# Kernel tuning notes

Measured on AMD Instinct MI355X. Metric: run time of the kernel, lower is better.

## Reference

```python
import jax, jax.numpy as jnp
import numpy as np

N = 400_000      # total nodes in batched graph
E = 6_400_000    # total edges (avg degree 16)
G = 6_400        # total small graphs
B = 64           # samples; num[i] graphs per sample, sum(num)=G
F = 31           # feature dim (hard-coded in TAG)
K = 2            # TAGConv hops
L = 5            # number of TAGConv layers
MAXG = 120       # max graphs per sample (120*31 pad)


def setup_inputs() -> dict:
    key = jax.random.key(0)
    ks = jax.random.split(key, 8)
    x = jax.random.normal(ks[0], (N, F), dtype=jnp.float32)
    src = jax.random.randint(ks[1], (E,), 0, N, dtype=jnp.int32)
    dst = jax.random.randint(ks[2], (E,), 0, N, dtype=jnp.int32)
    # contiguous (sorted) graph assignment, every graph non-empty (~62 nodes each)
    graph_ids = jnp.asarray((np.arange(N, dtype=np.int64) * G) // N, dtype=jnp.int32)
    num = jnp.full((B,), G // B, dtype=jnp.int32)  # 100 graphs per sample
    Ws = jax.random.normal(ks[3], (L, (K + 1) * F, F), dtype=jnp.float32) * 0.1
    bs = jax.random.normal(ks[4], (L, F), dtype=jnp.float32) * 0.01
    w_gate = jax.random.normal(ks[5], (F,), dtype=jnp.float32) * 0.1
    b_gate = jax.random.normal(ks[6], (1,), dtype=jnp.float32) * 0.01
    return {"x": x, "Ws": Ws, "bs": bs, "w_gate": w_gate, "b_gate": b_gate,
            "src": src, "dst": dst, "graph_ids": graph_ids, "num": num}


def reference(x, Ws, bs, w_gate, b_gate, src, dst, graph_ids, num):
    # symmetric normalization: norm = in_deg^{-1/2}, deg clamped to >=1 (DGL TAGConv)
    deg = jax.ops.segment_sum(jnp.ones((E,), x.dtype), dst, num_segments=N)
    norm = jnp.clip(deg, 1.0, None) ** -0.5  # [N]

    def tagconv(h, W, b):
        fstack = [h]
        cur = h
        for _ in range(K):
            cur = norm[:, None] * cur
            cur = jax.ops.segment_sum(cur[src], dst, num_segments=N)  # SPMM hop
            cur = norm[:, None] * cur
            fstack.append(cur)
        return jnp.concatenate(fstack, axis=-1) @ W + b  # [N, F]

    h = x
    for l in range(L):
        h = jax.nn.relu(tagconv(h, Ws[l], bs[l]))

    # GlobalAttentionPooling: segment softmax over gate scores, weighted sum
    gate = h @ w_gate + b_gate[0]                                   # [N]
    gmax = jax.ops.segment_max(gate, graph_ids, num_segments=G)     # [G]
    e = jnp.exp(gate - gmax[graph_ids])
    den = jax.ops.segment_sum(e, graph_ids, num_segments=G)
    alpha = e / den[graph_ids]
    rep = jax.ops.segment_sum(alpha[:, None] * h, graph_ids, num_segments=G)  # [G, F]

    # split by num, flatten, pad to 120*31, stack
    csum = jnp.cumsum(num)
    offsets = jnp.concatenate([jnp.zeros((1,), jnp.int32), csum.astype(jnp.int32)])
    g = jnp.arange(G, dtype=jnp.int32)
    sample_id = jnp.searchsorted(csum, g, side="right").astype(jnp.int32)  # [G]
    pos = g - offsets[sample_id]
    out = jnp.zeros((B, MAXG, F), rep.dtype).at[sample_id, pos].set(rep)
    return out.reshape(B, MAXG * F)
```

## Files before the change

### kernel.cpp

```cpp
#include <hip/hip_runtime.h>
#include <hip/hip_bf16.h>

#define FDIM 31
#define FPAD 32
#define RSTRIDE 16

#define CBITS 11
#define CW    (1 << CBITS)
#define MAXBUK 256
#define TILE 4096

typedef int      iv4 __attribute__((ext_vector_type(4)));
typedef unsigned uv4 __attribute__((ext_vector_type(4)));

__device__ __forceinline__ float bf_lo(unsigned u) { return __uint_as_float(u << 16); }
__device__ __forceinline__ float bf_hi(unsigned u) { return __uint_as_float(u & 0xFFFF0000u); }
__device__ __forceinline__ unsigned pack2(float lo, float hi) {
    unsigned a = __float_as_uint(lo), b = __float_as_uint(hi);
    unsigned ra = (a + 0x7FFFu + ((a >> 16) & 1u)) >> 16;
    unsigned rb = (b + 0x7FFFu + ((b >> 16) & 1u)) >> 16;
    return ra | (rb << 16);
}

__device__ __forceinline__ int lb_gid(const int* __restrict__ gid, int Ntot, int g) {
    int lo = 0, hi = Ntot;
    while (lo < hi) { int mid = (lo + hi) >> 1; if (gid[mid] < g) lo = mid + 1; else hi = mid; }
    return lo;
}

__global__ __launch_bounds__(256) void multisplit_kernel(
    const int* __restrict__ src, const int* __restrict__ dst,
    int* __restrict__ gcnt, int* __restrict__ bucketed,
    int cap, int E, int nbuk)
{
    __shared__ int ordered[TILE];
    __shared__ int hist[MAXBUK];
    __shared__ int lofs[MAXBUK + 1];
    __shared__ int base_[MAXBUK];
    __shared__ int cur[MAXBUK];
    const int tid = threadIdx.x;
    const int e0 = blockIdx.x * TILE;
    const int n = min(TILE, E - e0);
    if (tid < MAXBUK) hist[tid] = 0;
    __syncthreads();
    for (int i = tid; i < n; i += 256)
        atomicAdd(&hist[dst[e0 + i] >> CBITS], 1);
    __syncthreads();
    if (tid == 0) {
        int a = 0;
        for (int b = 0; b < nbuk; ++b) { lofs[b] = a; a += hist[b]; }
        lofs[nbuk] = a;
    }
    __syncthreads();
    if (tid < nbuk) {
        int h = hist[tid];
        base_[tid] = h ? atomicAdd(&gcnt[tid], h) : 0;
        cur[tid] = lofs[tid];
    }
    __syncthreads();
    for (int i = tid; i < n; i += 256) {
        int s = src[e0 + i], d = dst[e0 + i];
        int b = d >> CBITS;
        int r = atomicAdd(&cur[b], 1);
        ordered[r] = (s << CBITS) | (d & (CW - 1));
    }
    __syncthreads();
    for (int i = tid; i < n; i += 256) {
        int lo = 0, hi = nbuk;
        while (hi - lo > 1) {
            int mid = (lo + hi) >> 1;
            if (lofs[mid] <= i) lo = mid; else hi = mid;
        }
        int b = lo;
        int pos = base_[b] + (i - lofs[b]);
        if (pos < cap) bucketed[(size_t)b * cap + pos] = ordered[i];
    }
}

__global__ void small_scans_kernel(const int* __restrict__ num, int* __restrict__ soff, int Bn,
                                   const int* __restrict__ gcnt, int* __restrict__ bbase,
                                   int nbuk, int cap) {
    if (threadIdx.x == 0 && blockIdx.x == 0) {
        int acc = 0; soff[0] = 0;
        for (int i = 0; i < Bn; ++i) { acc += num[i]; soff[i + 1] = acc; }
        int a = 0;
        for (int b = 0; b < nbuk; ++b) {
            bbase[b] = a;
            a += ((min(gcnt[b], cap) + 7) & ~7) + 7 * CW;
        }
    }
}

__global__ __launch_bounds__(1024) void bucket_build_kernel(
    const int* __restrict__ bucketed, const int* __restrict__ gcnt,
    const int* __restrict__ bbase,
    int* __restrict__ rowbeg, int* __restrict__ rowend,
    float* __restrict__ normv, float* __restrict__ invn,
    int* __restrict__ col,
    int cap, int N, int nbuk)
{
    __shared__ int hist[CW];
    __shared__ int lcur[CW];
    const int b = blockIdx.x, tid = threadIdx.x;
    hist[tid] = 0; hist[tid + 1024] = 0;
    __syncthreads();
    const int cnt = min(gcnt[b], cap);
    const int* reg = bucketed + (size_t)b * cap;
    for (int i = tid; i < cnt; i += 1024)
        atomicAdd(&hist[reg[i] & (CW - 1)], 1);
    __syncthreads();
    int c0 = hist[tid], c1 = hist[tid + 1024];
    int p0 = (c0 + 7) & ~7, p1 = (c1 + 7) & ~7;
    __syncthreads();
    hist[tid] = p0; hist[tid + 1024] = p1;
    __syncthreads();
    for (int off = 1; off < CW; off <<= 1) {
        int a0 = (tid >= off) ? hist[tid - off] : 0;
        int a1 = (tid + 1024 >= off) ? hist[tid + 1024 - off] : 0;
        __syncthreads();
        hist[tid] += a0; hist[tid + 1024] += a1;
        __syncthreads();
    }
    const int base = bbase[b];
    const int base_node = b << CBITS;
    int r0 = -1, r1 = -1;
    int node = base_node + tid;
    if (node < N) {
        r0 = base + hist[tid] - p0;
        rowbeg[node] = r0; rowend[node] = r0 + p0; lcur[tid] = r0;
        int cr = c0 > 0 ? c0 : 1;
        normv[node] = rsqrtf((float)cr);
        invn[node]  = sqrtf((float)cr);
    }
    node = base_node + tid + 1024;
    if (node < N) {
        r1 = base + hist[tid + 1024] - p1;
        rowbeg[node] = r1; rowend[node] = r1 + p1; lcur[tid + 1024] = r1;
        int cr = c1 > 0 ? c1 : 1;
        normv[node] = rsqrtf((float)cr);
        invn[node]  = sqrtf((float)cr);
    }
    __syncthreads();
    for (int i = tid; i < cnt; i += 1024) {
        int e = reg[i];
        int p = atomicAdd(&lcur[e & (CW - 1)], 1);
        col[p] = e >> CBITS;
    }
    if (r0 >= 0) for (int j = r0 + c0; j < r0 + p0; ++j) col[j] = N;
    if (r1 >= 0) for (int j = r1 + c1; j < r1 + p1; ++j) col[j] = N;
}

__global__ void cast_x_kernel(const float* __restrict__ x, const float* __restrict__ normv,
                              unsigned* __restrict__ A, int N) {
    int idx = blockIdx.x * 256 + threadIdx.x;
    if (idx >= (N + 1) * RSTRIDE) return;
    int n = idx >> 4, q = idx & 15;
    if (n >= N) { A[idx] = 0u; return; }
    float nv = normv[n];
    int f0 = 2 * q, f1 = 2 * q + 1;
    float lo = (f0 < FDIM) ? nv * x[(size_t)n * FDIM + f0] : 0.0f;
    float hi = (f1 < FDIM) ? nv * x[(size_t)n * FDIM + f1] : 0.0f;
    A[idx] = pack2(lo, hi);
}

#define GATHER8(HSRC, r0, r1, r2, r3, r4, r5, r6, r7, CA, CB)                    \
    r0 = *((const uint4*)(HSRC + (size_t)(CA).x * RSTRIDE) + sub);               \
    r1 = *((const uint4*)(HSRC + (size_t)(CA).y * RSTRIDE) + sub);               \
    r2 = *((const uint4*)(HSRC + (size_t)(CA).z * RSTRIDE) + sub);               \
    r3 = *((const uint4*)(HSRC + (size_t)(CA).w * RSTRIDE) + sub);               \
    r4 = *((const uint4*)(HSRC + (size_t)(CB).x * RSTRIDE) + sub);               \
    r5 = *((const uint4*)(HSRC + (size_t)(CB).y * RSTRIDE) + sub);               \
    r6 = *((const uint4*)(HSRC + (size_t)(CB).z * RSTRIDE) + sub);               \
    r7 = *((const uint4*)(HSRC + (size_t)(CB).w * RSTRIDE) + sub);

#define ACC_EDGE(vN)                                                   \
    acc0 += bf_lo(vN.x); acc1 += bf_hi(vN.x);                          \
    acc2 += bf_lo(vN.y); acc3 += bf_hi(vN.y);                          \
    acc4 += bf_lo(vN.z); acc5 += bf_hi(vN.z);                          \
    acc6 += bf_lo(vN.w); acc7 += bf_hi(vN.w);

#define ACC8(r0, r1, r2, r3, r4, r5, r6, r7)                           \
    ACC_EDGE(r0) ACC_EDGE(r1) ACC_EDGE(r2) ACC_EDGE(r3)                \
    ACC_EDGE(r4) ACC_EDGE(r5) ACC_EDGE(r6) ACC_EDGE(r7)

__global__ __launch_bounds__(256) void spmm_kernel(const unsigned* __restrict__ Hin,
                                                   unsigned* __restrict__ Hout,
                                                   const int* __restrict__ rowbeg,
                                                   const int* __restrict__ rowend,
                                                   const int* __restrict__ col,
                                                   const float* __restrict__ normv, int N) {
    int node = blockIdx.x * 64 + (threadIdx.x >> 2);
    int sub = threadIdx.x & 3;
    if (node > N) return;
    if (node == N) {
        uv4 z = (uv4)0;
        __builtin_nontemporal_store(z, (uv4*)(Hout + (size_t)N * RSTRIDE) + sub);
        return;
    }
    int s = rowbeg[node];
    int nit = (rowend[node] - s) >> 3;
    float acc0 = 0.f, acc1 = 0.f, acc2 = 0.f, acc3 = 0.f;
    float acc4 = 0.f, acc5 = 0.f, acc6 = 0.f, acc7 = 0.f;
    if (nit > 0) {
        const iv4* cl = (const iv4*)(col + s);
        iv4 ca = __builtin_nontemporal_load(cl);
        iv4 cb = __builtin_nontemporal_load(cl + 1);
        for (int it = 0; it < nit; ++it) {
            uint4 v0, v1, v2, v3, v4, v5, v6, v7;
            GATHER8(Hin, v0, v1, v2, v3, v4, v5, v6, v7, ca, cb)
            const iv4* nx = cl + ((it + 1 < nit) ? 2 : 0);
            iv4 na = __builtin_nontemporal_load(nx);
            iv4 nb = __builtin_nontemporal_load(nx + 1);
            cl += 2;
            ACC8(v0, v1, v2, v3, v4, v5, v6, v7)
            ca = na; cb = nb;
        }
    }
    float nv = normv[node];
    float nn2 = nv * nv;
    uv4 o;
    o.x = pack2(nn2 * acc0, nn2 * acc1);
    o.y = pack2(nn2 * acc2, nn2 * acc3);
    o.z = pack2(nn2 * acc4, nn2 * acc5);
    o.w = pack2(nn2 * acc6, nn2 * acc7);
    __builtin_nontemporal_store(o, (uv4*)(Hout + (size_t)node * RSTRIDE) + sub);
}

__global__ __launch_bounds__(256, 5) void spmm_mlp_kernel(
    const unsigned* __restrict__ Hb,
    unsigned* __restrict__ Ha,
    const int* __restrict__ rowbeg,
    const int* __restrict__ rowend,
    const int* __restrict__ col,
    const float* __restrict__ normv,
    const float* __restrict__ invn,
    const float* __restrict__ W,
    const float* __restrict__ bias,
    float* __restrict__ gatev,
    const float* __restrict__ w_gate,
    const float* __restrict__ b_gate,
    int do_gate, int N)
{
    __shared__ float hcL[64 * 33];
    const int tid = threadIdx.x;
    {
        int node = blockIdx.x * 64 + (tid >> 2);
        int sub = tid & 3;
        if (node < N) {
            int s = rowbeg[node];
            int nit = (rowend[node] - s) >> 3;
            float acc0 = 0.f, acc1 = 0.f, acc2 = 0.f, acc3 = 0.f;
            float acc4 = 0.f, acc5 = 0.f, acc6 = 0.f, acc7 = 0.f;
            if (nit > 0) {
                const iv4* cl = (const iv4*)(col + s);
                iv4 ca = __builtin_nontemporal_load(cl);
                iv4 cb = __builtin_nontemporal_load(cl + 1);
                for (int it = 0; it < nit; ++it) {
                    uint4 v0, v1, v2, v3, v4, v5, v6, v7;
                    GATHER8(Hb, v0, v1, v2, v3, v4, v5, v6, v7, ca, cb)
                    const iv4* nx = cl + ((it + 1 < nit) ? 2 : 0);
                    iv4 na = __builtin_nontemporal_load(nx);
                    iv4 nb = __builtin_nontemporal_load(nx + 1);
                    cl += 2;
                    ACC8(v0, v1, v2, v3, v4, v5, v6, v7)
                    ca = na; cb = nb;
                }
            }
            float nv = normv[node];
            float nn2 = nv * nv;
            float* hp = &hcL[(tid >> 2) * 33 + sub * 8];
            hp[0] = nn2 * acc0; hp[1] = nn2 * acc1;
            hp[2] = nn2 * acc2; hp[3] = nn2 * acc3;
            hp[4] = nn2 * acc4; hp[5] = nn2 * acc5;
            hp[6] = nn2 * acc6; hp[7] = nn2 * acc7;
        }
    }
    __syncthreads();
    if (tid >= 64) return;
    int n2 = blockIdx.x * 64 + tid;
    if (n2 >= N) return;
    float out[FDIM];
#pragma unroll
    for (int j = 0; j < FDIM; ++j) out[j] = 0.0f;
#pragma unroll 1
    for (int blk = 0; blk < 2; ++blk) {
        const unsigned* bp = blk ? Hb : Ha;
        const uint4* r4p = (const uint4*)(bp + (size_t)n2 * RSTRIDE);
        uint4 r4[4];
#pragma unroll
        for (int q = 0; q < 4; ++q) r4[q] = r4p[q];
        const unsigned* ru = (const unsigned*)r4;
        const float* Wb = W + blk * FDIM * FDIM;
#pragma unroll
        for (int i = 0; i < FDIM; ++i) {
            float v = (i & 1) ? bf_hi(ru[i >> 1]) : bf_lo(ru[i >> 1]);
#pragma unroll
            for (int j = 0; j < FDIM; ++j) out[j] = fmaf(v, Wb[i * FDIM + j], out[j]);
        }
    }
    {
        const float* hp = &hcL[tid * 33];
        const float* W2 = W + 2 * FDIM * FDIM;
#pragma unroll
        for (int i = 0; i < FDIM; ++i) {
            float v = hp[i];
#pragma unroll
            for (int j = 0; j < FDIM; ++j) out[j] = fmaf(v, W2[i * FDIM + j], out[j]);
        }
    }
    float inv = invn[n2];
#pragma unroll
    for (int j = 0; j < FDIM; ++j) out[j] = fmaxf(fmaf(out[j], inv, bias[j]), 0.0f);
    float sc = do_gate ? 1.0f : normv[n2];
    unsigned* o = Ha + (size_t)n2 * RSTRIDE;
    uint4 w0, w1, w2, w3;
    w0.x = pack2(sc * out[0], sc * out[1]);   w0.y = pack2(sc * out[2], sc * out[3]);
    w0.z = pack2(sc * out[4], sc * out[5]);   w0.w = pack2(sc * out[6], sc * out[7]);
    w1.x = pack2(sc * out[8], sc * out[9]);   w1.y = pack2(sc * out[10], sc * out[11]);
    w1.z = pack2(sc * out[12], sc * out[13]); w1.w = pack2(sc * out[14], sc * out[15]);
    w2.x = pack2(sc * out[16], sc * out[17]); w2.y = pack2(sc * out[18], sc * out[19]);
    w2.z = pack2(sc * out[20], sc * out[21]); w2.w = pack2(sc * out[22], sc * out[23]);
    w3.x = pack2(sc * out[24], sc * out[25]); w3.y = pack2(sc * out[26], sc * out[27]);
    w3.z = pack2(sc * out[28], sc * out[29]); w3.w = pack2(sc * out[30], 0.0f);
    ((uint4*)o)[0] = w0; ((uint4*)o)[1] = w1; ((uint4*)o)[2] = w2; ((uint4*)o)[3] = w3;
    if (do_gate) {
        float g = b_gate[0];
#pragma unroll
        for (int j = 0; j < FDIM; ++j) g = fmaf(out[j], w_gate[j], g);
        gatev[n2] = g;
    }
}


__global__ __launch_bounds__(64) void graph_reduce_kernel(const float* __restrict__ gate,
                                                          const int* __restrict__ gid,
                                                          const int* __restrict__ soff, int Bn,
                                                          int Ntot,
                                                          float* __restrict__ gmax,
                                                          float* __restrict__ gden) {
    int g = blockIdx.x;
    if (g >= soff[Bn]) return;
    int s = lb_gid(gid, Ntot, g), e = lb_gid(gid, Ntot, g + 1);
    float m = -1e30f;
    for (int n = s + threadIdx.x; n < e; n += 64) m = fmaxf(m, gate[n]);
#pragma unroll
    for (int o = 32; o > 0; o >>= 1) m = fmaxf(m, __shfl_xor(m, o));
    float d = 0.0f;
    for (int n = s + threadIdx.x; n < e; n += 64) d += expf(gate[n] - m);
#pragma unroll
    for (int o = 32; o > 0; o >>= 1) d += __shfl_xor(d, o);
    if (threadIdx.x == 0) { gmax[g] = m; gden[g] = d; }
}

__global__ __launch_bounds__(64) void rep_scatter_kernel(const unsigned short* __restrict__ H,
                                                         const float* __restrict__ gate,
                                                         const int* __restrict__ gid,
                                                         const int* __restrict__ soff,
                                                         int MAXG, int Ntot,
                                                         const float* __restrict__ gmax,
                                                         const float* __restrict__ gden,
                                                         float* __restrict__ out) {
    int s = blockIdx.x / MAXG;
    int pos = blockIdx.x % MAXG;
    int t = threadIdx.x;
    if (t >= FDIM) return;
    int gbeg = soff[s], gend = soff[s + 1];
    float* op = out + ((size_t)s * MAXG + pos) * FDIM + t;
    if (pos >= gend - gbeg) { *op = 0.0f; return; }
    int g = gbeg + pos;
    int ns = lb_gid(gid, Ntot, g), ne = lb_gid(gid, Ntot, g + 1);
    float m = gmax[g], den = gden[g];
    float acc = 0.0f;
    for (int n = ns; n < ne; ++n) {
        float hv = __uint_as_float((unsigned)H[(size_t)n * FPAD + t] << 16);
        acc += expf(gate[n] - m) * hv;
    }
    *op = acc / den;
}


extern "C" void kernel_launch(void* const* d_in, const int* in_sizes, int n_in,
                              void* d_out, int out_size, void* d_ws, size_t ws_size,
                              hipStream_t stream) {
    const float* x      = (const float*)d_in[0];
    const float* Ws     = (const float*)d_in[1];
    const float* bs     = (const float*)d_in[2];
    const float* w_gate = (const float*)d_in[3];
    const float* b_gate = (const float*)d_in[4];
    const int* src       = (const int*)d_in[5];
    const int* dst       = (const int*)d_in[6];
    const int* graph_ids = (const int*)d_in[7];
    const int* num       = (const int*)d_in[8];
    float* out  = (float*)d_out;

    const int N  = in_sizes[7];
    const int E  = in_sizes[5];
    const int Bn = in_sizes[8];
    const int F  = in_sizes[3];
    const int L  = in_sizes[2] / F;
    const int nW = in_sizes[1];
    const int WperL = nW / L;
    const int MAXG = out_size / (Bn * F);
    const int Gmax = Bn * MAXG;

    const int nbuk = (N + CW - 1) / CW;
    const int cap  = E / nbuk + E / (8 * nbuk) + 2048;

    char* p = (char*)d_ws;
    auto alloc = [&](size_t bytes) {
        void* r = (void*)p;
        p += (bytes + 255) & ~(size_t)255;
        return r;
    };
    unsigned* HA = (unsigned*)alloc((size_t)(N + 1) * RSTRIDE * 4);
    unsigned* HB = (unsigned*)alloc((size_t)(N + 1) * RSTRIDE * 4);
    int*   colw  = (int*)alloc(((size_t)E + (size_t)nbuk * (7 * CW + 16)) * 4);
    int*   bkt   = (int*)alloc((size_t)nbuk * cap * 4);
    int*   gcnt  = (int*)alloc((size_t)nbuk * 4);
    int*   bbase = (int*)alloc((size_t)nbuk * 4);
    int*   rowb  = (int*)alloc((size_t)(N + 1) * 4);
    int*   rowe  = (int*)alloc((size_t)(N + 1) * 4);
    float* normv = (float*)alloc((size_t)N * 4);
    float* invnv = (float*)alloc((size_t)N * 4);
    float* gatev = (float*)alloc((size_t)N * 4);
    float* gmax  = (float*)alloc((size_t)Gmax * 4);
    float* gden  = (float*)alloc((size_t)Gmax * 4);
    int*   soff  = (int*)alloc((size_t)(Bn + 1) * 4);

    (void)hipMemsetAsync(gcnt, 0, (size_t)nbuk * 4, stream);

    const int NT = (E + TILE - 1) / TILE;
    multisplit_kernel<<<NT, 256, 0, stream>>>(src, dst, gcnt, bkt, cap, E, nbuk);
    small_scans_kernel<<<1, 64, 0, stream>>>(num, soff, Bn, gcnt, bbase, nbuk, cap);
    bucket_build_kernel<<<nbuk, 1024, 0, stream>>>(bkt, gcnt, bbase, rowb, rowe,
                                                   normv, invnv, colw, cap, N, nbuk);

    cast_x_kernel<<<((N + 1) * RSTRIDE + 255) / 256, 256, 0, stream>>>(x, normv, HA, N);

    const int SB  = (N + 1 + 63) / 64;
    const int SB2 = (N + 63) / 64;
    for (int l = 0; l < L; ++l) {
        spmm_kernel<<<SB, 256, 0, stream>>>(HA, HB, rowb, rowe, colw, normv, N);
        spmm_mlp_kernel<<<SB2, 256, 0, stream>>>(HB, HA, rowb, rowe, colw, normv, invnv,
                                                 Ws + (size_t)l * WperL, bs + (size_t)l * F,
                                                 gatev, w_gate, b_gate,
                                                 (l == L - 1) ? 1 : 0, N);
    }

    graph_reduce_kernel<<<Gmax, 64, 0, stream>>>(gatev, graph_ids, soff, Bn, N, gmax, gden);
    rep_scatter_kernel<<<Gmax, 64, 0, stream>>>((const unsigned short*)HA, gatev, graph_ids,
                                                soff, MAXG, N, gmax, gden, out);
    (void)n_in; (void)ws_size;
}
```

Measured before the change: 1.612 ms.

## Split per-node dense MLP across all four waves by output-column slices

The dense 93x31 transform after the SpMM gather previously ran on only the first wave of each 256-thread block, leaving three waves idle. Each wave now computes an 8-column slice of the output for the same 64 nodes and writes one 16-byte chunk of the bf16 row. The gate dot product is reduced across waves through shared memory. An extra barrier is added so the old Ha row is read before any wave overwrites it, and each wave reloads its own input rows.

```diff
diff --git a/kernel.cpp b/kernel.cpp
--- a/kernel.cpp
+++ b/kernel.cpp
@@ -242,6 +242,7 @@
     int do_gate, int N)
 {
     __shared__ float hcL[64 * 33];
+    __shared__ float gred[256];
     const int tid = threadIdx.x;
     {
         int node = blockIdx.x * 64 + (tid >> 2);
@@ -276,58 +277,91 @@
         }
     }
     __syncthreads();
-    if (tid >= 64) return;
-    int n2 = blockIdx.x * 64 + tid;
-    if (n2 >= N) return;
-    float out[FDIM];
-#pragma unroll
-    for (int j = 0; j < FDIM; ++j) out[j] = 0.0f;
-#pragma unroll 1
-    for (int blk = 0; blk < 2; ++blk) {
-        const unsigned* bp = blk ? Hb : Ha;
-        const uint4* r4p = (const uint4*)(bp + (size_t)n2 * RSTRIDE);
-        uint4 r4[4];
-#pragma unroll
-        for (int q = 0; q < 4; ++q) r4[q] = r4p[q];
-        const unsigned* ru = (const unsigned*)r4;
-        const float* Wb = W + blk * FDIM * FDIM;
-#pragma unroll
-        for (int i = 0; i < FDIM; ++i) {
-            float v = (i & 1) ? bf_hi(ru[i >> 1]) : bf_lo(ru[i >> 1]);
-#pragma unroll
-            for (int j = 0; j < FDIM; ++j) out[j] = fmaf(v, Wb[i * FDIM + j], out[j]);
-        }
-    }
-    {
-        const float* hp = &hcL[tid * 33];
-        const float* W2 = W + 2 * FDIM * FDIM;
-#pragma unroll
-        for (int i = 0; i < FDIM; ++i) {
-            float v = hp[i];
-#pragma unroll
-            for (int j = 0; j < FDIM; ++j) out[j] = fmaf(v, W2[i * FDIM + j], out[j]);
-        }
-    }
-    float inv = invn[n2];
-#pragma unroll
-    for (int j = 0; j < FDIM; ++j) out[j] = fmaxf(fmaf(out[j], inv, bias[j]), 0.0f);
-    float sc = do_gate ? 1.0f : normv[n2];
-    unsigned* o = Ha + (size_t)n2 * RSTRIDE;
-    uint4 w0, w1, w2, w3;
-    w0.x = pack2(sc * out[0], sc * out[1]);   w0.y = pack2(sc * out[2], sc * out[3]);
-    w0.z = pack2(sc * out[4], sc * out[5]);   w0.w = pack2(sc * out[6], sc * out[7]);
-    w1.x = pack2(sc * out[8], sc * out[9]);   w1.y = pack2(sc * out[10], sc * out[11]);
-    w1.z = pack2(sc * out[12], sc * out[13]); w1.w = pack2(sc * out[14], sc * out[15]);
-    w2.x = pack2(sc * out[16], sc * out[17]); w2.y = pack2(sc * out[18], sc * out[19]);
-    w2.z = pack2(sc * out[20], sc * out[21]); w2.w = pack2(sc * out[22], sc * out[23]);
-    w3.x = pack2(sc * out[24], sc * out[25]); w3.y = pack2(sc * out[26], sc * out[27]);
-    w3.z = pack2(sc * out[28], sc * out[29]); w3.w = pack2(sc * out[30], 0.0f);
-    ((uint4*)o)[0] = w0; ((uint4*)o)[1] = w1; ((uint4*)o)[2] = w2; ((uint4*)o)[3] = w3;
+    const int ln = tid & 63;
+    const int n2 = blockIdx.x * 64 + ln;
+    const int jb = __builtin_amdgcn_readfirstlane((tid >> 6) * 8);
+    uint4 ra[4];
+    if (n2 < N) {
+        const uint4* r4p = (const uint4*)(Ha + (size_t)n2 * RSTRIDE);
+#pragma unroll
+        for (int q = 0; q < 4; ++q) ra[q] = r4p[q];
+    }
+    __syncthreads();
+    float gp = 0.0f;
+    if (n2 < N) {
+        float out[8];
+#pragma unroll
+        for (int jj = 0; jj < 8; ++jj) out[jj] = 0.0f;
+        {
+            const unsigned* ru = (const unsigned*)ra;
+            const float* Wb = W;
+#pragma unroll
+            for (int i = 0; i < FDIM; ++i) {
+                float v = (i & 1) ? bf_hi(ru[i >> 1]) : bf_lo(ru[i >> 1]);
+#pragma unroll
+                for (int jj = 0; jj < 8; ++jj) {
+                    int j = jb + jj; j = j < FDIM ? j : FDIM - 1;
+                    out[jj] = fmaf(v, Wb[i * FDIM + j], out[jj]);
+                }
+            }
+        }
+        {
+            uint4 rb[4];
+            const uint4* r4p = (const uint4*)(Hb + (size_t)n2 * RSTRIDE);
+#pragma unroll
+            for (int q = 0; q < 4; ++q) rb[q] = r4p[q];
+            const unsigned* ru = (const unsigned*)rb;
+            const float* Wb = W + FDIM * FDIM;
+#pragma unroll
+            for (int i = 0; i < FDIM; ++i) {
+                float v = (i & 1) ? bf_hi(ru[i >> 1]) : bf_lo(ru[i >> 1]);
+#pragma unroll
+                for (int jj = 0; jj < 8; ++jj) {
+                    int j = jb + jj; j = j < FDIM ? j : FDIM - 1;
+                    out[jj] = fmaf(v, Wb[i * FDIM + j], out[jj]);
+                }
+            }
+        }
+        {
+            const float* hp = &hcL[ln * 33];
+            const float* Wb = W + 2 * FDIM * FDIM;
+#pragma unroll
+            for (int i = 0; i < FDIM; ++i) {
+                float v = hp[i];
+#pragma unroll
+                for (int jj = 0; jj < 8; ++jj) {
+                    int j = jb + jj; j = j < FDIM ? j : FDIM - 1;
+                    out[jj] = fmaf(v, Wb[i * FDIM + j], out[jj]);
+                }
+            }
+        }
+        float inv = invn[n2];
+#pragma unroll
+        for (int jj = 0; jj < 8; ++jj) {
+            int j = jb + jj; j = j < FDIM ? j : FDIM - 1;
+            out[jj] = fmaxf(fmaf(out[jj], inv, bias[j]), 0.0f);
+        }
+        if (jb + 7 >= FDIM) out[7] = 0.0f;
+        float sc = do_gate ? 1.0f : normv[n2];
+        uint4 q;
+        q.x = pack2(sc * out[0], sc * out[1]);
+        q.y = pack2(sc * out[2], sc * out[3]);
+        q.z = pack2(sc * out[4], sc * out[5]);
+        q.w = pack2(sc * out[6], sc * out[7]);
+        ((uint4*)(Ha + (size_t)n2 * RSTRIDE))[jb >> 3] = q;
+        if (do_gate) {
+#pragma unroll
+            for (int jj = 0; jj < 8; ++jj) {
+                int j = jb + jj; j = j < FDIM ? j : FDIM - 1;
+                gp = fmaf(out[jj], w_gate[j], gp);
+            }
+        }
+    }
     if (do_gate) {
-        float g = b_gate[0];
-#pragma unroll
-        for (int j = 0; j < FDIM; ++j) g = fmaf(out[j], w_gate[j], g);
-        gatev[n2] = g;
+        gred[tid] = gp;
+        __syncthreads();
+        if (tid < 64 && n2 < N)
+            gatev[n2] = b_gate[0] + gred[tid] + gred[tid + 64] + gred[tid + 128] + gred[tid + 192];
     }
 }
 
```

After: 1.956 ms. +21.4%, slower.
